# Performance work log

Hardware: AMD Instinct MI355X
Metric: run time of the kernel (lower is better)

The kernel has to match this reference:

```python
import jax, jax.numpy as jnp
import numpy as np
import math

NUM_HEADS = 16
HEAD_DIM = 64  # 1024 / 16

def setup_inputs() -> dict:
    key = jax.random.key(0)
    k1, k2, k3 = jax.random.split(key, 3)
    B, S, D = 2, 2048, 1024
    scale = 1.0 / math.sqrt(D)
    return {
        "hidden_states": jax.random.normal(k1, (B, S, D), dtype=jnp.float32),
        "attention_mask": jnp.ones((B, S), dtype=jnp.int32),
        "Wq": jax.random.normal(k2, (D, D), dtype=jnp.float32) * scale,
        "bq": jnp.zeros((D,), dtype=jnp.float32),
        "Wk": jax.random.normal(k3, (D, D), dtype=jnp.float32) * scale,
        "bk": jnp.zeros((D,), dtype=jnp.float32),
    }

def _split_heads(x):
    # [B, S, D] -> [B, H, S, dh]
    B, S, D = x.shape
    return x.reshape(B, S, NUM_HEADS, HEAD_DIM).transpose(0, 2, 1, 3)

def reference(hidden_states, attention_mask, Wq, bq, Wk, bk):
    q = _split_heads(hidden_states @ Wq + bq)           # [B,H,S,dh]
    k = _split_heads(hidden_states @ Wk + bk)           # [B,H,S,dh]
    k = jax.nn.log_sigmoid(q) + q + k                   # fused logsigmoid on q
    k = jax.nn.log_sigmoid(k)                           # second logsigmoid
    # scores = q @ (-k^T) / sqrt(dh)
    scores = -jnp.einsum('bhqd,bhkd->bhqk', q, k) / math.sqrt(HEAD_DIM)
    # mask broadcast [B,1,S,1]: masks QUERY rows (faithful to original)
    mask = (attention_mask[:, None, :, None] == 0)
    scores = jnp.where(mask, -10000.0, scores)
    probs = jax.nn.softmax(scores, axis=-1)             # [B,H,S,S]
    # note: value == query_layer in this module
    ctx = jnp.einsum('bhqk,bhkd->bhqd', probs, q)       # [B,H,S,dh]
    B, H, S, dh = ctx.shape
    return ctx.transpose(0, 2, 1, 3).reshape(B, S, H * dh)
```

## Files before the change

kernel.cpp:

```cpp
#include <hip/hip_runtime.h>
#include <hip/hip_bf16.h>
#include <math.h>

#define B_  2
#define S_  2048
#define D_  1024
#define H_  16
#define DH_ 64
#define M_  (B_ * S_)

typedef __attribute__((ext_vector_type(8))) short bf16x8;
typedef __attribute__((ext_vector_type(4))) float f32x4;
typedef __attribute__((ext_vector_type(16))) float f32x16;
typedef __attribute__((ext_vector_type(2))) unsigned u32x2;

__device__ __forceinline__ float fast_exp2(float x) {
  return __builtin_amdgcn_exp2f(x);
}

__device__ __forceinline__ unsigned short f2bf(float f) {
  union { float f; unsigned u; } c; c.f = f;
  unsigned u = c.u;
  return (unsigned short)((u + 0x7FFFu + ((u >> 16) & 1u)) >> 16);
}

__device__ __forceinline__ unsigned cvtpk(float lo, float hi) {
  unsigned r;
  asm("v_cvt_pk_bf16_f32 %0, %1, %2" : "=v"(r) : "v"(lo), "v"(hi));
  return r;
}

__device__ __forceinline__ void plswap(unsigned &x, unsigned &y) {
  u32x2 r = __builtin_amdgcn_permlane32_swap(x, y, false, false);
  x = r[0]; y = r[1];
}

__device__ __forceinline__ float logsig(float x) {
  const float e = __expf(-fabsf(x));
  return fminf(x, 0.f) - __logf(1.f + e);
}

__global__ __launch_bounds__(256) void prep_w(
    const float* __restrict__ Wq, const float* __restrict__ Wk,
    unsigned short* __restrict__ WqT, unsigned short* __restrict__ WkT)
{
  __shared__ unsigned short T[64][72];
  const int tid = threadIdx.x;
  const int k0 = blockIdx.x * 64;
  const int n0 = blockIdx.y * 64;
  const float* W = blockIdx.z ? Wk : Wq;
  unsigned short* WT = blockIdx.z ? WkT : WqT;

  const int kr = tid >> 2, nc = (tid & 3) * 16;
  #pragma unroll
  for (int i = 0; i < 4; i++) {
    const float4 v = *(const float4*)&W[(size_t)(k0 + kr) * D_ + n0 + nc + i * 4];
    T[nc + i * 4 + 0][kr] = f2bf(v.x);
    T[nc + i * 4 + 1][kr] = f2bf(v.y);
    T[nc + i * 4 + 2][kr] = f2bf(v.z);
    T[nc + i * 4 + 3][kr] = f2bf(v.w);
  }
  __syncthreads();
  const int nr = tid >> 2, kc = (tid & 3) * 16;
  const uint4 a = *(const uint4*)&T[nr][kc];
  const uint4 b = *(const uint4*)&T[nr][kc + 8];
  *(uint4*)&WT[(size_t)(n0 + nr) * D_ + k0 + kc] = a;
  *(uint4*)&WT[(size_t)(n0 + nr) * D_ + k0 + kc + 8] = b;
}

__global__ __launch_bounds__(512, 4) void proj_kernel(
    const float* __restrict__ hs,
    const unsigned short* __restrict__ WqT, const unsigned short* __restrict__ WkT,
    const float* __restrict__ bqv, const float* __restrict__ bkv,
    unsigned short* __restrict__ K2b, unsigned short* __restrict__ QT)
{
  __shared__ unsigned short Ash[128][72];
  __shared__ unsigned short Bsh[2][64][72];

  const int tid  = threadIdx.x;
  const int w    = tid >> 6;
  const int lane = tid & 63;
  const int r31  = lane & 31;
  const int hi   = lane >> 5;
  const int hi8  = hi * 8;
  const int msel = w & 3;
  const int nsel = w >> 2;
  const int m0 = blockIdx.x * 128;
  const int n0 = blockIdx.y * 64;

  const int n_loc = nsel * 32 + r31;
  const float bqs = bqv[n0 + n_loc];
  const float bks = bkv[n0 + n_loc];

  f32x16 accQ, accK;
  #pragma unroll
  for (int r = 0; r < 16; r++) { accQ[r] = 0.f; accK[r] = 0.f; }

  const int am = tid >> 2, ac = (tid & 3) * 16;
  const int bn = tid >> 3, bc = (tid & 7) * 8;

  float4 Af[4];
  uint4 Bq, Bk;
  {
    const size_t ra = (size_t)(m0 + am) * D_ + ac;
    #pragma unroll
    for (int i = 0; i < 4; i++) Af[i] = *(const float4*)&hs[ra + i * 4];
    const size_t rb = (size_t)(n0 + bn) * D_ + bc;
    Bq = *(const uint4*)&WqT[rb];
    Bk = *(const uint4*)&WkT[rb];
  }

  for (int k0 = 0; k0 < D_; k0 += 64) {
    if (k0) __syncthreads();
    {
      uint4 t0, t1;
      t0.x = cvtpk(Af[0].x, Af[0].y);  t0.y = cvtpk(Af[0].z, Af[0].w);
      t0.z = cvtpk(Af[1].x, Af[1].y);  t0.w = cvtpk(Af[1].z, Af[1].w);
      t1.x = cvtpk(Af[2].x, Af[2].y);  t1.y = cvtpk(Af[2].z, Af[2].w);
      t1.z = cvtpk(Af[3].x, Af[3].y);  t1.w = cvtpk(Af[3].z, Af[3].w);
      *(uint4*)&Ash[am][ac]     = t0;
      *(uint4*)&Ash[am][ac + 8] = t1;
    }
    *(uint4*)&Bsh[0][bn][bc] = Bq;
    *(uint4*)&Bsh[1][bn][bc] = Bk;
    __syncthreads();

    if (k0 + 64 < D_) {
      const size_t ra = (size_t)(m0 + am) * D_ + (k0 + 64) + ac;
      #pragma unroll
      for (int i = 0; i < 4; i++) Af[i] = *(const float4*)&hs[ra + i * 4];
      const size_t rb = (size_t)(n0 + bn) * D_ + (k0 + 64) + bc;
      Bq = *(const uint4*)&WqT[rb];
      Bk = *(const uint4*)&WkT[rb];
    }

    __builtin_amdgcn_s_setprio(1);
    #pragma unroll
    for (int s = 0; s < 4; s++) {
      const bf16x8 af  = *(const bf16x8*)&Ash[msel * 32 + r31][s * 16 + hi8];
      const bf16x8 bqf = *(const bf16x8*)&Bsh[0][nsel * 32 + r31][s * 16 + hi8];
      const bf16x8 bkf = *(const bf16x8*)&Bsh[1][nsel * 32 + r31][s * 16 + hi8];
      accQ = __builtin_amdgcn_mfma_f32_32x32x16_bf16(af, bqf, accQ, 0, 0, 0);
      accK = __builtin_amdgcn_mfma_f32_32x32x16_bf16(af, bkf, accK, 0, 0, 0);
    }
    __builtin_amdgcn_s_setprio(0);
  }
  __syncthreads();

  unsigned short* Qt = &Bsh[0][0][0];
  float qv[16];
  #pragma unroll
  for (int r = 0; r < 16; r++) {
    const float q  = accQ[r] + bqs;
    const float kr = accK[r] + bks;
    const float k2 = logsig(logsig(q) + q + kr);
    const int m = m0 + msel * 32 + (r & 3) + 8 * (r >> 2) + 4 * hi;
    K2b[(size_t)m * D_ + n0 + n_loc] = f2bf(k2);
    qv[r] = q;
  }
  #pragma unroll
  for (int rq = 0; rq < 4; rq++) {
    const ushort4 qu = {f2bf(qv[4*rq]), f2bf(qv[4*rq+1]),
                        f2bf(qv[4*rq+2]), f2bf(qv[4*rq+3])};
    *(ushort4*)&Qt[n_loc * 136 + msel * 32 + rq * 8 + 4 * hi] = qu;
  }
  __syncthreads();
  {
    const int dr = tid >> 3, mc = (tid & 7) * 16;
    #pragma unroll
    for (int i = 0; i < 2; i++) {
      const uint4 v = *(const uint4*)&Qt[dr * 136 + mc + i * 8];
      *(uint4*)&QT[(size_t)(n0 + dr) * M_ + m0 + mc + i * 8] = v;
    }
  }
}

__global__ __launch_bounds__(1024) void attn_kernel(
    const unsigned short* __restrict__ QT,
    const unsigned short* __restrict__ K2b,
    const int* __restrict__ mask,
    float* __restrict__ out)
{
  __shared__ unsigned short Qa [256][72];
  __shared__ unsigned short K2s[64][72];
  __shared__ unsigned short Vt [64][72];

  const int tid  = threadIdx.x;
  const int w    = tid >> 6;
  const int lane = tid & 63;
  const int r31  = lane & 31;
  const int hi   = lane >> 5;
  const int hi8  = hi * 8;
  const int qsub = w & 7;
  const int ksel = w >> 3;

  const int qt = blockIdx.x;
  const int bh = blockIdx.y;
  const int b = bh >> 4, h = bh & 15;
  const size_t qrow0 = (size_t)b * S_ + (size_t)qt * 256;
  const size_t krow0 = (size_t)b * S_;
  const size_t trow  = (size_t)h * 64;

  const int rr = tid >> 4, cc = (tid & 15) * 4;
  uint2 kreg, vreg;
  kreg = *(const uint2*)&K2b[(krow0 + rr) * D_ + trow + cc];
  vreg = *(const uint2*)&QT [(trow + rr) * M_ + krow0 + cc];

  {
    const int dr = tid >> 4, qg = tid & 15;
    const int qc = qg * 16;
    const int dcol = dr ^ ((qg & 7) << 3);
    #pragma unroll
    for (int i = 0; i < 2; i++) {
      const uint4 v = *(const uint4*)&QT[(trow + dr) * M_ + qrow0 + qc + i * 8];
      const unsigned short* p = (const unsigned short*)&v;
      #pragma unroll
      for (int j = 0; j < 8; j++) Qa[qc + i * 8 + j][dcol] = p[j];
    }
  }
  __syncthreads();

  bf16x8 qfrag[4];
  {
    const int qrow = qsub * 32 + r31;
    const int g7 = (qrow >> 4) & 7;
    #pragma unroll
    for (int s = 0; s < 4; s++)
      qfrag[s] = *(const bf16x8*)&Qa[qrow][(s * 16 + hi8) ^ (g7 << 3)];
  }

  const float c2 = (mask[qrow0 + qsub * 32 + r31] != 0) ? -0.18033688f : 0.f;
  float rl = 0.f;

  f32x16 Ot0, Ot1;
  #pragma unroll
  for (int r = 0; r < 16; r++) { Ot0[r] = 0.f; Ot1[r] = 0.f; }

  const int NT = S_ / 64;
  for (int kt = 0; kt < NT; kt++) {
    __syncthreads();
    *(uint2*)&K2s[rr][cc] = kreg;
    *(uint2*)&Vt [rr][cc] = vreg;
    __syncthreads();

    if (kt + 1 < NT) {
      kreg = *(const uint2*)&K2b[(krow0 + (kt + 1) * 64 + rr) * D_ + trow + cc];
      vreg = *(const uint2*)&QT [(trow + rr) * M_ + krow0 + (kt + 1) * 64 + cc];
    }

    bf16x8 kf[4];
    #pragma unroll
    for (int s = 0; s < 4; s++)
      kf[s] = *(const bf16x8*)&K2s[ksel * 32 + r31][s * 16 + hi8];
    f32x16 sc;
    #pragma unroll
    for (int r = 0; r < 16; r++) sc[r] = 0.f;
    __builtin_amdgcn_s_setprio(1);
    #pragma unroll
    for (int s = 0; s < 4; s++)
      sc = __builtin_amdgcn_mfma_f32_32x32x16_bf16(kf[s], qfrag[s], sc, 0, 0, 0);
    __builtin_amdgcn_s_setprio(0);

    float p[16];
    #pragma unroll
    for (int r = 0; r < 16; r++) p[r] = fast_exp2(fmaf(sc[r], c2, -12.f));
    #pragma unroll
    for (int r = 0; r < 16; r += 4) rl += ((p[r] + p[r+1]) + (p[r+2] + p[r+3]));

    unsigned pk0 = cvtpk(p[0],  p[1]),  pk1 = cvtpk(p[2],  p[3]);
    unsigned pk2 = cvtpk(p[4],  p[5]),  pk3 = cvtpk(p[6],  p[7]);
    unsigned pk4 = cvtpk(p[8],  p[9]),  pk5 = cvtpk(p[10], p[11]);
    unsigned pk6 = cvtpk(p[12], p[13]), pk7 = cvtpk(p[14], p[15]);
    plswap(pk0, pk2);
    plswap(pk1, pk3);
    plswap(pk4, pk6);
    plswap(pk5, pk7);
    union { unsigned d[8]; bf16x8 v[2]; } pu;
    pu.d[0] = pk0; pu.d[1] = pk1; pu.d[2] = pk2; pu.d[3] = pk3;
    pu.d[4] = pk4; pu.d[5] = pk5; pu.d[6] = pk6; pu.d[7] = pk7;

    __builtin_amdgcn_s_setprio(1);
    #pragma unroll
    for (int s2 = 0; s2 < 2; s2++) {
      const bf16x8 pf  = pu.v[s2];
      const bf16x8 vf0 = *(const bf16x8*)&Vt[r31]     [ksel * 32 + s2 * 16 + hi8];
      const bf16x8 vf1 = *(const bf16x8*)&Vt[32 + r31][ksel * 32 + s2 * 16 + hi8];
      Ot0 = __builtin_amdgcn_mfma_f32_32x32x16_bf16(vf0, pf, Ot0, 0, 0, 0);
      Ot1 = __builtin_amdgcn_mfma_f32_32x32x16_bf16(vf1, pf, Ot1, 0, 0, 0);
    }
    __builtin_amdgcn_s_setprio(0);
  }

  rl += __shfl_xor(rl, 32);
  __syncthreads();
  float* redO = (float*)&Qa[0][0];
  float* redL = (float*)&K2s[0][0];
  if (ksel == 1) {
    #pragma unroll
    for (int r = 0; r < 16; r++) redO[(qsub * 16 + r) * 64 + lane] = Ot0[r];
    redL[qsub * 64 + lane] = rl;
  }
  __syncthreads();
  float inv = 0.f;
  size_t orow = 0;
  if (ksel == 0) {
    const float lt = rl + redL[qsub * 64 + lane];
    inv = 1.f / fmaxf(lt, 1e-35f);
    orow = (qrow0 + qsub * 32 + r31) * D_ + trow;
    #pragma unroll
    for (int rq = 0; rq < 4; rq++) {
      float4 o;
      o.x = (Ot0[4*rq+0] + redO[(qsub*16 + 4*rq+0)*64 + lane]) * inv;
      o.y = (Ot0[4*rq+1] + redO[(qsub*16 + 4*rq+1)*64 + lane]) * inv;
      o.z = (Ot0[4*rq+2] + redO[(qsub*16 + 4*rq+2)*64 + lane]) * inv;
      o.w = (Ot0[4*rq+3] + redO[(qsub*16 + 4*rq+3)*64 + lane]) * inv;
      *(float4*)&out[orow + rq * 8 + 4 * hi] = o;
    }
  }
  __syncthreads();
  if (ksel == 1) {
    #pragma unroll
    for (int r = 0; r < 16; r++) redO[(qsub * 16 + r) * 64 + lane] = Ot1[r];
  }
  __syncthreads();
  if (ksel == 0) {
    #pragma unroll
    for (int rq = 0; rq < 4; rq++) {
      float4 o;
      o.x = (Ot1[4*rq+0] + redO[(qsub*16 + 4*rq+0)*64 + lane]) * inv;
      o.y = (Ot1[4*rq+1] + redO[(qsub*16 + 4*rq+1)*64 + lane]) * inv;
      o.z = (Ot1[4*rq+2] + redO[(qsub*16 + 4*rq+2)*64 + lane]) * inv;
      o.w = (Ot1[4*rq+3] + redO[(qsub*16 + 4*rq+3)*64 + lane]) * inv;
      *(float4*)&out[orow + 32 + rq * 8 + 4 * hi] = o;
    }
  }
}

extern "C" void kernel_launch(void* const* d_in, const int* in_sizes, int n_in,
                              void* d_out, int out_size, void* d_ws, size_t ws_size,
                              hipStream_t stream) {
  const float* hs  = (const float*)d_in[0];
  const int*   msk = (const int*)d_in[1];
  const float* Wq  = (const float*)d_in[2];
  const float* bq  = (const float*)d_in[3];
  const float* Wk  = (const float*)d_in[4];
  const float* bk  = (const float*)d_in[5];
  float* out = (float*)d_out;

  unsigned short* QT  = (unsigned short*)d_ws;
  unsigned short* K2b = QT  + (size_t)D_ * M_;
  unsigned short* WqT = K2b + (size_t)M_ * D_;
  unsigned short* WkT = WqT + (size_t)D_ * D_;

  prep_w<<<dim3(D_ / 64, D_ / 64, 2), 256, 0, stream>>>(Wq, Wk, WqT, WkT);
  proj_kernel<<<dim3(M_ / 128, D_ / 64), 512, 0, stream>>>(hs, WqT, WkT, bq, bk, K2b, QT);
  attn_kernel<<<dim3(S_ / 256, B_ * H_), 1024, 0, stream>>>(QT, K2b, msk, out);
}
```

Measured before the change: 152.8 us.

## Enlarge proj M-tile to 256 and attention K-tile to 128 per sync

```diff
diff --git a/kernel.cpp b/kernel.cpp
--- a/kernel.cpp
+++ b/kernel.cpp
@@ -10,7 +10,6 @@
 #define M_  (B_ * S_)
 
 typedef __attribute__((ext_vector_type(8))) short bf16x8;
-typedef __attribute__((ext_vector_type(4))) float f32x4;
 typedef __attribute__((ext_vector_type(16))) float f32x16;
 typedef __attribute__((ext_vector_type(2))) unsigned u32x2;
 
@@ -68,13 +67,13 @@
   *(uint4*)&WT[(size_t)(n0 + nr) * D_ + k0 + kc + 8] = b;
 }
 
-__global__ __launch_bounds__(512, 4) void proj_kernel(
+__global__ __launch_bounds__(1024) void proj_kernel(
     const float* __restrict__ hs,
     const unsigned short* __restrict__ WqT, const unsigned short* __restrict__ WkT,
     const float* __restrict__ bqv, const float* __restrict__ bkv,
     unsigned short* __restrict__ K2b, unsigned short* __restrict__ QT)
 {
-  __shared__ unsigned short Ash[128][72];
+  __shared__ unsigned short Ash[256][72];
   __shared__ unsigned short Bsh[2][64][72];
 
   const int tid  = threadIdx.x;
@@ -83,9 +82,9 @@
   const int r31  = lane & 31;
   const int hi   = lane >> 5;
   const int hi8  = hi * 8;
-  const int msel = w & 3;
-  const int nsel = w >> 2;
-  const int m0 = blockIdx.x * 128;
+  const int msel = w & 7;
+  const int nsel = w >> 3;
+  const int m0 = blockIdx.x * 256;
   const int n0 = blockIdx.y * 64;
 
   const int n_loc = nsel * 32 + r31;
@@ -97,17 +96,17 @@
   for (int r = 0; r < 16; r++) { accQ[r] = 0.f; accK[r] = 0.f; }
 
   const int am = tid >> 2, ac = (tid & 3) * 16;
-  const int bn = tid >> 3, bc = (tid & 7) * 8;
+  const int bn = tid >> 4, bc = (tid & 15) * 4;
 
   float4 Af[4];
-  uint4 Bq, Bk;
+  uint2 Bq, Bk;
   {
     const size_t ra = (size_t)(m0 + am) * D_ + ac;
     #pragma unroll
     for (int i = 0; i < 4; i++) Af[i] = *(const float4*)&hs[ra + i * 4];
     const size_t rb = (size_t)(n0 + bn) * D_ + bc;
-    Bq = *(const uint4*)&WqT[rb];
-    Bk = *(const uint4*)&WkT[rb];
+    Bq = *(const uint2*)&WqT[rb];
+    Bk = *(const uint2*)&WkT[rb];
   }
 
   for (int k0 = 0; k0 < D_; k0 += 64) {
@@ -121,8 +120,8 @@
       *(uint4*)&Ash[am][ac]     = t0;
       *(uint4*)&Ash[am][ac + 8] = t1;
     }
-    *(uint4*)&Bsh[0][bn][bc] = Bq;
-    *(uint4*)&Bsh[1][bn][bc] = Bk;
+    *(uint2*)&Bsh[0][bn][bc] = Bq;
+    *(uint2*)&Bsh[1][bn][bc] = Bk;
     __syncthreads();
 
     if (k0 + 64 < D_) {
@@ -130,8 +129,8 @@
       #pragma unroll
       for (int i = 0; i < 4; i++) Af[i] = *(const float4*)&hs[ra + i * 4];
       const size_t rb = (size_t)(n0 + bn) * D_ + (k0 + 64) + bc;
-      Bq = *(const uint4*)&WqT[rb];
-      Bk = *(const uint4*)&WkT[rb];
+      Bq = *(const uint2*)&WqT[rb];
+      Bk = *(const uint2*)&WkT[rb];
     }
 
     __builtin_amdgcn_s_setprio(1);
@@ -145,9 +144,7 @@
     }
     __builtin_amdgcn_s_setprio(0);
   }
-  __syncthreads();
-
-  unsigned short* Qt = &Bsh[0][0][0];
+
   float qv[16];
   #pragma unroll
   for (int r = 0; r < 16; r++) {
@@ -162,16 +159,7 @@
   for (int rq = 0; rq < 4; rq++) {
     const ushort4 qu = {f2bf(qv[4*rq]), f2bf(qv[4*rq+1]),
                         f2bf(qv[4*rq+2]), f2bf(qv[4*rq+3])};
-    *(ushort4*)&Qt[n_loc * 136 + msel * 32 + rq * 8 + 4 * hi] = qu;
-  }
-  __syncthreads();
-  {
-    const int dr = tid >> 3, mc = (tid & 7) * 16;
-    #pragma unroll
-    for (int i = 0; i < 2; i++) {
-      const uint4 v = *(const uint4*)&Qt[dr * 136 + mc + i * 8];
-      *(uint4*)&QT[(size_t)(n0 + dr) * M_ + m0 + mc + i * 8] = v;
-    }
+    *(ushort4*)&QT[(size_t)(n0 + n_loc) * M_ + m0 + msel * 32 + rq * 8 + 4 * hi] = qu;
   }
 }
 
@@ -182,8 +170,8 @@
     float* __restrict__ out)
 {
   __shared__ unsigned short Qa [256][72];
-  __shared__ unsigned short K2s[64][72];
-  __shared__ unsigned short Vt [64][72];
+  __shared__ unsigned short K2s[128][72];
+  __shared__ unsigned short Vt [64][136];
 
   const int tid  = threadIdx.x;
   const int w    = tid >> 6;
@@ -201,10 +189,11 @@
   const size_t krow0 = (size_t)b * S_;
   const size_t trow  = (size_t)h * 64;
 
-  const int rr = tid >> 4, cc = (tid & 15) * 4;
-  uint2 kreg, vreg;
-  kreg = *(const uint2*)&K2b[(krow0 + rr) * D_ + trow + cc];
-  vreg = *(const uint2*)&QT [(trow + rr) * M_ + krow0 + cc];
+  const int krr = tid >> 3, kcc = (tid & 7) * 8;
+  const int vrr = tid >> 4, vcc = (tid & 15) * 8;
+  uint4 kreg, vreg;
+  kreg = *(const uint4*)&K2b[(krow0 + krr) * D_ + trow + kcc];
+  vreg = *(const uint4*)&QT [(trow + vrr) * M_ + krow0 + vcc];
 
   {
     const int dr = tid >> 4, qg = tid & 15;
@@ -236,59 +225,64 @@
   #pragma unroll
   for (int r = 0; r < 16; r++) { Ot0[r] = 0.f; Ot1[r] = 0.f; }
 
-  const int NT = S_ / 64;
+  const int NT = S_ / 128;
   for (int kt = 0; kt < NT; kt++) {
     __syncthreads();
-    *(uint2*)&K2s[rr][cc] = kreg;
-    *(uint2*)&Vt [rr][cc] = vreg;
+    *(uint4*)&K2s[krr][kcc] = kreg;
+    *(uint4*)&Vt [vrr][vcc] = vreg;
     __syncthreads();
 
     if (kt + 1 < NT) {
-      kreg = *(const uint2*)&K2b[(krow0 + (kt + 1) * 64 + rr) * D_ + trow + cc];
-      vreg = *(const uint2*)&QT [(trow + rr) * M_ + krow0 + (kt + 1) * 64 + cc];
-    }
-
-    bf16x8 kf[4];
-    #pragma unroll
-    for (int s = 0; s < 4; s++)
-      kf[s] = *(const bf16x8*)&K2s[ksel * 32 + r31][s * 16 + hi8];
-    f32x16 sc;
-    #pragma unroll
-    for (int r = 0; r < 16; r++) sc[r] = 0.f;
-    __builtin_amdgcn_s_setprio(1);
-    #pragma unroll
-    for (int s = 0; s < 4; s++)
-      sc = __builtin_amdgcn_mfma_f32_32x32x16_bf16(kf[s], qfrag[s], sc, 0, 0, 0);
-    __builtin_amdgcn_s_setprio(0);
-
-    float p[16];
-    #pragma unroll
-    for (int r = 0; r < 16; r++) p[r] = fast_exp2(fmaf(sc[r], c2, -12.f));
-    #pragma unroll
-    for (int r = 0; r < 16; r += 4) rl += ((p[r] + p[r+1]) + (p[r+2] + p[r+3]));
-
-    unsigned pk0 = cvtpk(p[0],  p[1]),  pk1 = cvtpk(p[2],  p[3]);
-    unsigned pk2 = cvtpk(p[4],  p[5]),  pk3 = cvtpk(p[6],  p[7]);
-    unsigned pk4 = cvtpk(p[8],  p[9]),  pk5 = cvtpk(p[10], p[11]);
-    unsigned pk6 = cvtpk(p[12], p[13]), pk7 = cvtpk(p[14], p[15]);
-    plswap(pk0, pk2);
-    plswap(pk1, pk3);
-    plswap(pk4, pk6);
-    plswap(pk5, pk7);
-    union { unsigned d[8]; bf16x8 v[2]; } pu;
-    pu.d[0] = pk0; pu.d[1] = pk1; pu.d[2] = pk2; pu.d[3] = pk3;
-    pu.d[4] = pk4; pu.d[5] = pk5; pu.d[6] = pk6; pu.d[7] = pk7;
-
-    __builtin_amdgcn_s_setprio(1);
-    #pragma unroll
-    for (int s2 = 0; s2 < 2; s2++) {
-      const bf16x8 pf  = pu.v[s2];
-      const bf16x8 vf0 = *(const bf16x8*)&Vt[r31]     [ksel * 32 + s2 * 16 + hi8];
-      const bf16x8 vf1 = *(const bf16x8*)&Vt[32 + r31][ksel * 32 + s2 * 16 + hi8];
-      Ot0 = __builtin_amdgcn_mfma_f32_32x32x16_bf16(vf0, pf, Ot0, 0, 0, 0);
-      Ot1 = __builtin_amdgcn_mfma_f32_32x32x16_bf16(vf1, pf, Ot1, 0, 0, 0);
-    }
-    __builtin_amdgcn_s_setprio(0);
+      kreg = *(const uint4*)&K2b[(krow0 + (kt + 1) * 128 + krr) * D_ + trow + kcc];
+      vreg = *(const uint4*)&QT [(trow + vrr) * M_ + krow0 + (kt + 1) * 128 + vcc];
+    }
+
+    #pragma unroll
+    for (int sub = 0; sub < 2; sub++) {
+      const int kb = sub * 64;
+
+      bf16x8 kf[4];
+      #pragma unroll
+      for (int s = 0; s < 4; s++)
+        kf[s] = *(const bf16x8*)&K2s[kb + ksel * 32 + r31][s * 16 + hi8];
+      f32x16 sc;
+      #pragma unroll
+      for (int r = 0; r < 16; r++) sc[r] = 0.f;
+      __builtin_amdgcn_s_setprio(1);
+      #pragma unroll
+      for (int s = 0; s < 4; s++)
+        sc = __builtin_amdgcn_mfma_f32_32x32x16_bf16(kf[s], qfrag[s], sc, 0, 0, 0);
+      __builtin_amdgcn_s_setprio(0);
+
+      float p[16];
+      #pragma unroll
+      for (int r = 0; r < 16; r++) p[r] = fast_exp2(fmaf(sc[r], c2, -12.f));
+      #pragma unroll
+      for (int r = 0; r < 16; r += 4) rl += ((p[r] + p[r+1]) + (p[r+2] + p[r+3]));
+
+      unsigned pk0 = cvtpk(p[0],  p[1]),  pk1 = cvtpk(p[2],  p[3]);
+      unsigned pk2 = cvtpk(p[4],  p[5]),  pk3 = cvtpk(p[6],  p[7]);
+      unsigned pk4 = cvtpk(p[8],  p[9]),  pk5 = cvtpk(p[10], p[11]);
+      unsigned pk6 = cvtpk(p[12], p[13]), pk7 = cvtpk(p[14], p[15]);
+      plswap(pk0, pk2);
+      plswap(pk1, pk3);
+      plswap(pk4, pk6);
+      plswap(pk5, pk7);
+      union { unsigned d[8]; bf16x8 v[2]; } pu;
+      pu.d[0] = pk0; pu.d[1] = pk1; pu.d[2] = pk2; pu.d[3] = pk3;
+      pu.d[4] = pk4; pu.d[5] = pk5; pu.d[6] = pk6; pu.d[7] = pk7;
+
+      __builtin_amdgcn_s_setprio(1);
+      #pragma unroll
+      for (int s2 = 0; s2 < 2; s2++) {
+        const bf16x8 pf  = pu.v[s2];
+        const bf16x8 vf0 = *(const bf16x8*)&Vt[r31]     [kb + ksel * 32 + s2 * 16 + hi8];
+        const bf16x8 vf1 = *(const bf16x8*)&Vt[32 + r31][kb + ksel * 32 + s2 * 16 + hi8];
+        Ot0 = __builtin_amdgcn_mfma_f32_32x32x16_bf16(vf0, pf, Ot0, 0, 0, 0);
+        Ot1 = __builtin_amdgcn_mfma_f32_32x32x16_bf16(vf1, pf, Ot1, 0, 0, 0);
+      }
+      __builtin_amdgcn_s_setprio(0);
+    }
   }
 
   rl += __shfl_xor(rl, 32);
@@ -353,6 +347,6 @@
   unsigned short* WkT = WqT + (size_t)D_ * D_;
 
   prep_w<<<dim3(D_ / 64, D_ / 64, 2), 256, 0, stream>>>(Wq, Wk, WqT, WkT);
-  proj_kernel<<<dim3(M_ / 128, D_ / 64), 512, 0, stream>>>(hs, WqT, WkT, bq, bk, K2b, QT);
+  proj_kernel<<<dim3(M_ / 256, D_ / 64), 1024, 0, stream>>>(hs, WqT, WkT, bq, bk, K2b, QT);
   attn_kernel<<<dim3(S_ / 256, B_ * H_), 1024, 0, stream>>>(QT, K2b, msk, out);
 }
```

New measurement: 158.2 us. 3.5% more time.

## Double key tile per barrier to 128 and remap blocks for L2 locality

Applied to the files above, without the earlier changes.

```diff
diff --git a/kernel.cpp b/kernel.cpp
--- a/kernel.cpp
+++ b/kernel.cpp
@@ -10,7 +10,6 @@
 #define M_  (B_ * S_)
 
 typedef __attribute__((ext_vector_type(8))) short bf16x8;
-typedef __attribute__((ext_vector_type(4))) float f32x4;
 typedef __attribute__((ext_vector_type(16))) float f32x16;
 typedef __attribute__((ext_vector_type(2))) unsigned u32x2;
 
@@ -182,8 +181,8 @@
     float* __restrict__ out)
 {
   __shared__ unsigned short Qa [256][72];
-  __shared__ unsigned short K2s[64][72];
-  __shared__ unsigned short Vt [64][72];
+  __shared__ unsigned short K2s[128][72];
+  __shared__ unsigned short Vt [64][136];
 
   const int tid  = threadIdx.x;
   const int w    = tid >> 6;
@@ -194,17 +193,19 @@
   const int qsub = w & 7;
   const int ksel = w >> 3;
 
-  const int qt = blockIdx.x;
-  const int bh = blockIdx.y;
+  const int lid = blockIdx.x + 8 * blockIdx.y;
+  const int bh  = (lid & 7) + 8 * (lid >> 6);
+  const int qt  = (lid >> 3) & 7;
   const int b = bh >> 4, h = bh & 15;
   const size_t qrow0 = (size_t)b * S_ + (size_t)qt * 256;
   const size_t krow0 = (size_t)b * S_;
   const size_t trow  = (size_t)h * 64;
 
-  const int rr = tid >> 4, cc = (tid & 15) * 4;
-  uint2 kreg, vreg;
-  kreg = *(const uint2*)&K2b[(krow0 + rr) * D_ + trow + cc];
-  vreg = *(const uint2*)&QT [(trow + rr) * M_ + krow0 + cc];
+  const int krr = tid >> 3, kcc = (tid & 7) * 8;
+  const int vrr = tid >> 4, vcc = (tid & 15) * 8;
+  uint4 kreg, vreg;
+  kreg = *(const uint4*)&K2b[(krow0 + krr) * D_ + trow + kcc];
+  vreg = *(const uint4*)&QT [(trow + vrr) * M_ + krow0 + vcc];
 
   {
     const int dr = tid >> 4, qg = tid & 15;
@@ -236,59 +237,64 @@
   #pragma unroll
   for (int r = 0; r < 16; r++) { Ot0[r] = 0.f; Ot1[r] = 0.f; }
 
-  const int NT = S_ / 64;
+  const int NT = S_ / 128;
   for (int kt = 0; kt < NT; kt++) {
     __syncthreads();
-    *(uint2*)&K2s[rr][cc] = kreg;
-    *(uint2*)&Vt [rr][cc] = vreg;
+    *(uint4*)&K2s[krr][kcc] = kreg;
+    *(uint4*)&Vt [vrr][vcc] = vreg;
     __syncthreads();
 
     if (kt + 1 < NT) {
-      kreg = *(const uint2*)&K2b[(krow0 + (kt + 1) * 64 + rr) * D_ + trow + cc];
-      vreg = *(const uint2*)&QT [(trow + rr) * M_ + krow0 + (kt + 1) * 64 + cc];
-    }
-
-    bf16x8 kf[4];
-    #pragma unroll
-    for (int s = 0; s < 4; s++)
-      kf[s] = *(const bf16x8*)&K2s[ksel * 32 + r31][s * 16 + hi8];
-    f32x16 sc;
-    #pragma unroll
-    for (int r = 0; r < 16; r++) sc[r] = 0.f;
-    __builtin_amdgcn_s_setprio(1);
-    #pragma unroll
-    for (int s = 0; s < 4; s++)
-      sc = __builtin_amdgcn_mfma_f32_32x32x16_bf16(kf[s], qfrag[s], sc, 0, 0, 0);
-    __builtin_amdgcn_s_setprio(0);
-
-    float p[16];
-    #pragma unroll
-    for (int r = 0; r < 16; r++) p[r] = fast_exp2(fmaf(sc[r], c2, -12.f));
-    #pragma unroll
-    for (int r = 0; r < 16; r += 4) rl += ((p[r] + p[r+1]) + (p[r+2] + p[r+3]));
-
-    unsigned pk0 = cvtpk(p[0],  p[1]),  pk1 = cvtpk(p[2],  p[3]);
-    unsigned pk2 = cvtpk(p[4],  p[5]),  pk3 = cvtpk(p[6],  p[7]);
-    unsigned pk4 = cvtpk(p[8],  p[9]),  pk5 = cvtpk(p[10], p[11]);
-    unsigned pk6 = cvtpk(p[12], p[13]), pk7 = cvtpk(p[14], p[15]);
-    plswap(pk0, pk2);
-    plswap(pk1, pk3);
-    plswap(pk4, pk6);
-    plswap(pk5, pk7);
-    union { unsigned d[8]; bf16x8 v[2]; } pu;
-    pu.d[0] = pk0; pu.d[1] = pk1; pu.d[2] = pk2; pu.d[3] = pk3;
-    pu.d[4] = pk4; pu.d[5] = pk5; pu.d[6] = pk6; pu.d[7] = pk7;
-
-    __builtin_amdgcn_s_setprio(1);
-    #pragma unroll
-    for (int s2 = 0; s2 < 2; s2++) {
-      const bf16x8 pf  = pu.v[s2];
-      const bf16x8 vf0 = *(const bf16x8*)&Vt[r31]     [ksel * 32 + s2 * 16 + hi8];
-      const bf16x8 vf1 = *(const bf16x8*)&Vt[32 + r31][ksel * 32 + s2 * 16 + hi8];
-      Ot0 = __builtin_amdgcn_mfma_f32_32x32x16_bf16(vf0, pf, Ot0, 0, 0, 0);
-      Ot1 = __builtin_amdgcn_mfma_f32_32x32x16_bf16(vf1, pf, Ot1, 0, 0, 0);
-    }
-    __builtin_amdgcn_s_setprio(0);
+      kreg = *(const uint4*)&K2b[(krow0 + (kt + 1) * 128 + krr) * D_ + trow + kcc];
+      vreg = *(const uint4*)&QT [(trow + vrr) * M_ + krow0 + (kt + 1) * 128 + vcc];
+    }
+
+    #pragma unroll
+    for (int sub = 0; sub < 2; sub++) {
+      const int kb = sub * 64;
+
+      bf16x8 kf[4];
+      #pragma unroll
+      for (int s = 0; s < 4; s++)
+        kf[s] = *(const bf16x8*)&K2s[kb + ksel * 32 + r31][s * 16 + hi8];
+      f32x16 sc;
+      #pragma unroll
+      for (int r = 0; r < 16; r++) sc[r] = 0.f;
+      __builtin_amdgcn_s_setprio(1);
+      #pragma unroll
+      for (int s = 0; s < 4; s++)
+        sc = __builtin_amdgcn_mfma_f32_32x32x16_bf16(kf[s], qfrag[s], sc, 0, 0, 0);
+      __builtin_amdgcn_s_setprio(0);
+
+      float p[16];
+      #pragma unroll
+      for (int r = 0; r < 16; r++) p[r] = fast_exp2(fmaf(sc[r], c2, -12.f));
+      #pragma unroll
+      for (int r = 0; r < 16; r += 4) rl += ((p[r] + p[r+1]) + (p[r+2] + p[r+3]));
+
+      unsigned pk0 = cvtpk(p[0],  p[1]),  pk1 = cvtpk(p[2],  p[3]);
+      unsigned pk2 = cvtpk(p[4],  p[5]),  pk3 = cvtpk(p[6],  p[7]);
+      unsigned pk4 = cvtpk(p[8],  p[9]),  pk5 = cvtpk(p[10], p[11]);
+      unsigned pk6 = cvtpk(p[12], p[13]), pk7 = cvtpk(p[14], p[15]);
+      plswap(pk0, pk2);
+      plswap(pk1, pk3);
+      plswap(pk4, pk6);
+      plswap(pk5, pk7);
+      union { unsigned d[8]; bf16x8 v[2]; } pu;
+      pu.d[0] = pk0; pu.d[1] = pk1; pu.d[2] = pk2; pu.d[3] = pk3;
+      pu.d[4] = pk4; pu.d[5] = pk5; pu.d[6] = pk6; pu.d[7] = pk7;
+
+      __builtin_amdgcn_s_setprio(1);
+      #pragma unroll
+      for (int s2 = 0; s2 < 2; s2++) {
+        const bf16x8 pf  = pu.v[s2];
+        const bf16x8 vf0 = *(const bf16x8*)&Vt[r31]     [kb + ksel * 32 + s2 * 16 + hi8];
+        const bf16x8 vf1 = *(const bf16x8*)&Vt[32 + r31][kb + ksel * 32 + s2 * 16 + hi8];
+        Ot0 = __builtin_amdgcn_mfma_f32_32x32x16_bf16(vf0, pf, Ot0, 0, 0, 0);
+        Ot1 = __builtin_amdgcn_mfma_f32_32x32x16_bf16(vf1, pf, Ot1, 0, 0, 0);
+      }
+      __builtin_amdgcn_s_setprio(0);
+    }
   }
 
   rl += __shfl_xor(rl, 32);
```

Measured after the change: 148.6 us. -2.7%, faster.
